# Kernel optimization log

Hardware: AMD Instinct MI355X
Metric: run time of the kernel (lower is better)

The kernel has to match this reference:

```python
import jax, jax.numpy as jnp
import numpy as np
from jax import lax

EPS = 1e-5

def conv2d(x, w, b, pad):
    y = lax.conv_general_dilated(x, w, (1, 1), [(pad, pad), (pad, pad)],
                                 dimension_numbers=('NCHW', 'OIHW', 'NCHW'))
    return y + b[None, :, None, None]

def batchnorm(x, gamma, beta):
    mean = jnp.mean(x, axis=(0, 2, 3), keepdims=True)
    var = jnp.var(x, axis=(0, 2, 3), keepdims=True)  # biased, as torch BN training mode
    return gamma[None, :, None, None] * (x - mean) * lax.rsqrt(var + EPS) + beta[None, :, None, None]

def maxpool2(x):
    return lax.reduce_window(x, -jnp.inf, lax.max, (1, 1, 2, 2), (1, 1, 2, 2), 'VALID')

def upsample(x, s):
    N, C, H, W = x.shape
    return jax.image.resize(x, (N, C, H * s, W * s), method='bilinear')

def select_topvar(x, k=3):
    # per-sample, per-channel unbiased variance; gather top-k variance channels
    N, C, H, W = x.shape
    v = jnp.var(x.reshape(N, C, H * W), axis=-1, ddof=1)  # [N, C]
    _, idx = lax.top_k(v, k)                              # argsort(-v)[:k]
    return jnp.take_along_axis(x, idx[:, :, None, None], axis=1)

def setup_inputs() -> dict:
    key = jax.random.key(0)
    ks = jax.random.split(key, 16)
    n_channel, n_class = 10, 5
    d = {}
    d['x'] = jax.random.normal(ks[0], (16, n_channel, 512, 512), jnp.float32)
    sc = 0.1
    d['w_ext1'] = jax.random.normal(ks[1], (16, n_channel, 1, 1), jnp.float32) * sc
    d['b_ext1'] = jnp.zeros((16,), jnp.float32)
    d['g_ebn1'] = jnp.ones((16,), jnp.float32)
    d['be_ebn1'] = jnp.zeros((16,), jnp.float32)
    d['w_ext2'] = jax.random.normal(ks[2], (16, 16, 1, 1), jnp.float32) * sc
    d['b_ext2'] = jnp.zeros((16,), jnp.float32)
    d['g_ebn2'] = jnp.ones((16,), jnp.float32)
    d['be_ebn2'] = jnp.zeros((16,), jnp.float32)
    d['w_c1'] = jax.random.normal(ks[3], (8, 3, 3, 3), jnp.float32) * sc
    d['b_c1'] = jnp.zeros((8,), jnp.float32)
    d['w_c2'] = jax.random.normal(ks[4], (16, 8, 3, 3), jnp.float32) * sc
    d['b_c2'] = jnp.zeros((16,), jnp.float32)
    d['g_bn1'] = jnp.ones((16,), jnp.float32)
    d['be_bn1'] = jnp.zeros((16,), jnp.float32)
    d['g_bn2'] = jnp.ones((8,), jnp.float32)
    d['be_bn2'] = jnp.zeros((8,), jnp.float32)
    d['w_1k'] = jax.random.normal(ks[5], (n_class, 24, 1, 1), jnp.float32) * sc
    d['b_1k'] = jnp.zeros((n_class,), jnp.float32)
    return d

def reference(x, w_ext1, b_ext1, g_ebn1, be_ebn1, w_ext2, b_ext2, g_ebn2, be_ebn2,
              w_c1, b_c1, w_c2, b_c2, g_bn1, be_bn1, g_bn2, be_bn2, w_1k, b_1k):
    # bandExtract: 1x1 conv -> BN -> sigmoid, twice
    h = jax.nn.sigmoid(batchnorm(conv2d(x, w_ext1, b_ext1, 0), g_ebn1, be_ebn1))
    h = jax.nn.sigmoid(batchnorm(conv2d(h, w_ext2, b_ext2, 0), g_ebn2, be_ebn2))
    # featureSelect: keep 3 channels with largest per-sample variance
    x0 = select_topvar(h, 3)                                   # [N,3,H,W]
    x1 = maxpool2(jax.nn.sigmoid(conv2d(x0, w_c1, b_c1, 1)))   # [N,8,H/2,W/2]
    x2 = maxpool2(jax.nn.sigmoid(conv2d(x1, w_c2, b_c2, 1)))   # [N,16,H/4,W/4]
    x2 = batchnorm(jax.nn.relu(upsample(x2, 4)), g_bn1, be_bn1)  # [N,16,H,W]
    x1 = batchnorm(jax.nn.relu(upsample(x1, 2)), g_bn2, be_bn2)  # [N,8,H,W]
    merge = jnp.concatenate([x1, x2], axis=1)                    # [N,24,H,W]
    return conv2d(merge, w_1k, b_1k, 0)                          # [N,n_class,H,W]
```

## Files before the change

kernel.cpp:

```cpp
#include <hip/hip_runtime.h>
#include <math.h>

#define N_    16
#define CIN_  10
#define CB_   16
#define H_    512
#define W_    512
#define HW_   (512*512)
#define EPSF  1e-5f

__device__ __forceinline__ float sgm(float z){
  float e = __builtin_amdgcn_exp2f(z * -1.44269504088896f);
  return __builtin_amdgcn_rcpf(1.0f + e);
}

__global__ void k_zero(double* __restrict__ p, int n){
  int i = blockIdx.x*256 + threadIdx.x;
  if (i < n) p[i] = 0.0;
}

__global__ void k_fin(const double* __restrict__ S, const float* __restrict__ g,
                      const float* __restrict__ be, float* __restrict__ AB,
                      int C, double invM){
  int c = threadIdx.x;
  if (c < C){
    double s=0.0,q=0.0;
    for (int n=0;n<N_;++n){ s+=S[(n*C+c)*2]; q+=S[(n*C+c)*2+1]; }
    double mean = s*invM;
    double var  = q*invM - mean*mean;
    float a = g[c]*rsqrtf((float)var + EPSF);
    AB[c]   = a;
    AB[C+c] = be[c] - (float)mean*a;
  }
}

__global__ __launch_bounds__(256) void k_cov(
    const float* __restrict__ x, double* __restrict__ SP)
{
  const int n = blockIdx.y;
  const int base = blockIdx.x*4096;
  const float* xp = x + (size_t)n*CIN_*HW_;
  float s[CIN_], p[55];
#pragma unroll
  for (int i=0;i<CIN_;++i) s[i]=0.f;
#pragma unroll
  for (int i=0;i<55;++i) p[i]=0.f;
#pragma unroll 1
  for (int it=0; it<4; ++it){
    const int off = base + it*1024 + threadIdx.x*4;
    float4 xv[CIN_];
#pragma unroll
    for (int ci=0; ci<CIN_; ++ci)
      xv[ci] = *(const float4*)(xp + (size_t)ci*HW_ + off);
#pragma unroll
    for (int ci=0; ci<CIN_; ++ci)
      s[ci] += xv[ci].x + xv[ci].y + xv[ci].z + xv[ci].w;
    int k=0;
#pragma unroll
    for (int i=0;i<CIN_;++i)
#pragma unroll
      for (int j=i;j<CIN_;++j,++k)
        p[k] += xv[i].x*xv[j].x + xv[i].y*xv[j].y + xv[i].z*xv[j].z + xv[i].w*xv[j].w;
  }
  __shared__ float red[4][65];
  const int lane = threadIdx.x & 63, wid = threadIdx.x >> 6;
#pragma unroll
  for (int k=0;k<65;++k){
    float v = (k<CIN_) ? s[k] : p[k-CIN_];
    for (int o=32;o>0;o>>=1) v += __shfl_down(v,o);
    if (lane==0) red[wid][k]=v;
  }
  __syncthreads();
  if (threadIdx.x < 65){
    float v = red[0][threadIdx.x]+red[1][threadIdx.x]+red[2][threadIdx.x]+red[3][threadIdx.x];
    atomicAdd(&SP[n*65+threadIdx.x], (double)v);
  }
}

__global__ void k_fin1(const double* __restrict__ SP, const float* __restrict__ w1,
                       const float* __restrict__ b1, const float* __restrict__ g,
                       const float* __restrict__ be, float* __restrict__ AB){
  __shared__ double Sm[CIN_], Cv[55];
  int t = threadIdx.x;
  if (t < 65){
    double s = 0.0;
    for (int n=0;n<N_;++n) s += SP[n*65+t];
    if (t < CIN_) Sm[t] = s; else Cv[t-CIN_] = s;
  }
  __syncthreads();
  if (t < CB_){
    const double M = 16.0*(double)HW_;
    double b = (double)b1[t];
    double wd[CIN_];
    double lin = 0.0;
    for (int i=0;i<CIN_;++i){ wd[i] = (double)w1[t*CIN_+i]; lin += wd[i]*Sm[i]/M; }
    double mean = b + lin;
    double ey2 = b*b + 2.0*b*lin;
    int k=0;
    for (int i=0;i<CIN_;++i)
      for (int j=i;j<CIN_;++j,++k)
        ey2 += (i==j ? 1.0 : 2.0) * wd[i]*wd[j]*(Cv[k]/M);
    double var = ey2 - mean*mean;
    float a = g[t]*rsqrtf((float)var + EPSF);
    AB[t] = a;
    AB[CB_+t] = be[t] - (float)mean*a;
  }
}

__global__ __launch_bounds__(256) void k_band2(
    const float* __restrict__ x,
    const float* __restrict__ w1, const float* __restrict__ b1, const float* __restrict__ AB1,
    const float* __restrict__ w2, const float* __restrict__ b2,
    float* __restrict__ B, double* __restrict__ S2)
{
  const int n = blockIdx.y;
  const int base = blockIdx.x*4096;
  const float* xp = x + (size_t)n*CIN_*HW_;
  float* bp = B + (size_t)n*CB_*HW_;
  float sum[CB_], sq[CB_];
#pragma unroll
  for (int c=0;c<CB_;++c){ sum[c]=0.f; sq[c]=0.f; }
#pragma unroll 1
  for (int it=0; it<4; ++it){
    const int p = base + it*1024 + threadIdx.x*4;
    float4 xv[CIN_];
#pragma unroll
    for (int ci=0; ci<CIN_; ++ci)
      xv[ci] = *(const float4*)(xp + (size_t)ci*HW_ + p);
    float4 s[CB_];
#pragma unroll
    for (int co=0; co<CB_; ++co){
      float bb = b1[co];
      float ox=bb, oy=bb, oz=bb, ow=bb;
#pragma unroll
      for (int ci=0; ci<CIN_; ++ci){
        float w = w1[co*CIN_+ci];
        ox += w*xv[ci].x; oy += w*xv[ci].y; oz += w*xv[ci].z; ow += w*xv[ci].w;
      }
      const float a = AB1[co], sh = AB1[CB_+co];
      s[co].x = sgm(a*ox+sh); s[co].y = sgm(a*oy+sh);
      s[co].z = sgm(a*oz+sh); s[co].w = sgm(a*ow+sh);
    }
#pragma unroll
    for (int co=0; co<CB_; ++co){
      float bb = b2[co];
      float ox=bb, oy=bb, oz=bb, ow=bb;
#pragma unroll
      for (int ci=0; ci<CB_; ++ci){
        float w = w2[co*CB_+ci];
        ox += w*s[ci].x; oy += w*s[ci].y; oz += w*s[ci].z; ow += w*s[ci].w;
      }
      float4 o; o.x=ox; o.y=oy; o.z=oz; o.w=ow;
      *(float4*)(bp + (size_t)co*HW_ + p) = o;
      sum[co] += ox+oy+oz+ow;
      sq[co]  += ox*ox+oy*oy+oz*oz+ow*ow;
    }
  }
  __shared__ float red[4][CB_][2];
  const int lane = threadIdx.x & 63, wid = threadIdx.x >> 6;
#pragma unroll
  for (int c=0;c<CB_;++c){
    float s=sum[c], q=sq[c];
    for (int off=32; off>0; off>>=1){ s += __shfl_down(s,off); q += __shfl_down(q,off); }
    if (lane==0){ red[wid][c][0]=s; red[wid][c][1]=q; }
  }
  __syncthreads();
  if (threadIdx.x < CB_*2){
    int c = threadIdx.x>>1, k = threadIdx.x&1;
    float t = red[0][c][k]+red[1][c][k]+red[2][c][k]+red[3][c][k];
    atomicAdd(&S2[(n*CB_+c)*2+k], (double)t);
  }
}

__global__ __launch_bounds__(256) void k_varstats(
    const float* __restrict__ B, const float* __restrict__ AB2, double* __restrict__ SV)
{
  const int n = blockIdx.z, c = blockIdx.y;
  const float a = AB2[c], b = AB2[CB_+c];
  const float* p = B + ((size_t)(n*CB_+c))*HW_ + blockIdx.x*4096;
  float sum=0.f, sq=0.f;
#pragma unroll 1
  for (int it=0; it<4; ++it){
    float4 v = *(const float4*)(p + it*1024 + threadIdx.x*4);
    v.x = sgm(a*v.x+b); v.y = sgm(a*v.y+b); v.z = sgm(a*v.z+b); v.w = sgm(a*v.w+b);
    sum += v.x+v.y+v.z+v.w;
    sq  += v.x*v.x+v.y*v.y+v.z*v.z+v.w*v.w;
  }
  __shared__ float red[4][2];
  const int lane = threadIdx.x & 63, wid = threadIdx.x >> 6;
  for (int off=32; off>0; off>>=1){ sum += __shfl_down(sum,off); sq += __shfl_down(sq,off); }
  if (lane==0){ red[wid][0]=sum; red[wid][1]=sq; }
  __syncthreads();
  if (threadIdx.x < 2){
    int k = threadIdx.x;
    float t = red[0][k]+red[1][k]+red[2][k]+red[3][k];
    atomicAdd(&SV[(n*CB_+c)*2+k], (double)t);
  }
}

__global__ void k_topk(const double* __restrict__ SV, int* __restrict__ IDX){
  __shared__ double var[N_][CB_];
  int t = threadIdx.x;
  if (t < N_*CB_){
    int n=t>>4, c=t&15;
    double s=SV[t*2], q=SV[t*2+1];
    const double M = (double)HW_;
    var[n][c] = (q - s*s/M)/(M-1.0);
  }
  __syncthreads();
  if (t < N_){
    double v[CB_];
#pragma unroll
    for (int c=0;c<CB_;++c) v[c]=var[t][c];
    for (int k=0;k<3;++k){
      int bi=0; double bv=v[0];
#pragma unroll
      for (int c=1;c<CB_;++c) if (v[c]>bv){ bv=v[c]; bi=c; }
      IDX[t*3+k]=bi; v[bi]=-1e300;
    }
  }
}

__global__ __launch_bounds__(256) void k_conv1p(
    const float* __restrict__ B, const int* __restrict__ IDX, const float* __restrict__ AB2,
    const float* __restrict__ w, const float* __restrict__ bias,
    float* __restrict__ X1)
{
  const int n = blockIdx.y, ho = blockIdx.x, wo = threadIdx.x;
  __shared__ int chs[3];
  __shared__ float ca[3], cb[3];
  if (threadIdx.x < 3){
    int c = IDX[n*3+threadIdx.x];
    chs[threadIdx.x] = c;
    ca[threadIdx.x] = AB2[c];
    cb[threadIdx.x] = AB2[CB_+c];
  }
  __syncthreads();
  float in[3][4][4];
#pragma unroll
  for (int k=0;k<3;++k){
    const float* pc = B + ((size_t)(n*CB_+chs[k]))*HW_;
    const float a = ca[k], bb = cb[k];
#pragma unroll
    for (int dy=0;dy<4;++dy){
      int r = 2*ho-1+dy;
      bool rok = (r>=0 && r<H_);
#pragma unroll
      for (int dx=0;dx<4;++dx){
        int cc = 2*wo-1+dx;
        in[k][dy][dx] = (rok && cc>=0 && cc<W_) ? sgm(a*pc[(size_t)r*W_+cc]+bb) : 0.f;
      }
    }
  }
#pragma unroll
  for (int co=0;co<8;++co){
    float m = -1e30f;
#pragma unroll
    for (int py=0;py<2;++py)
#pragma unroll
    for (int px=0;px<2;++px){
      float acc = bias[co];
#pragma unroll
      for (int k=0;k<3;++k)
#pragma unroll
      for (int kh=0;kh<3;++kh)
#pragma unroll
      for (int kw=0;kw<3;++kw)
        acc += w[((co*3+k)*3+kh)*3+kw] * in[k][py+kh][px+kw];
      m = fmaxf(m, acc);
    }
    X1[((size_t)(n*8+co)*256 + ho)*256 + wo] = sgm(m);
  }
}

__global__ __launch_bounds__(256) void k_conv2p(
    const float* __restrict__ X1, const float* __restrict__ w, const float* __restrict__ bias,
    float* __restrict__ X2)
{
  const int n  = blockIdx.y;
  const int wo = threadIdx.x & 127;
  const int ho = blockIdx.x*2 + (threadIdx.x>>7);
  float acc[16][4];
#pragma unroll
  for (int co=0;co<16;++co){
    float bb = bias[co];
    acc[co][0]=bb; acc[co][1]=bb; acc[co][2]=bb; acc[co][3]=bb;
  }
#pragma unroll 1
  for (int ci=0; ci<8; ++ci){
    const float* p = X1 + ((size_t)(n*8+ci))*65536;
    float patch[4][4];
#pragma unroll
    for (int dy=0;dy<4;++dy){
      int r = 2*ho-1+dy;
      bool rok = (r>=0 && r<256);
#pragma unroll
      for (int dx=0;dx<4;++dx){
        int cc = 2*wo-1+dx;
        patch[dy][dx] = (rok && cc>=0 && cc<256) ? p[r*256+cc] : 0.f;
      }
    }
#pragma unroll
    for (int co=0;co<16;++co){
      const float* wp = w + (co*8+ci)*9;
#pragma unroll
      for (int py=0;py<2;++py)
#pragma unroll
      for (int px=0;px<2;++px){
        float a = acc[co][py*2+px];
#pragma unroll
        for (int kh=0;kh<3;++kh)
#pragma unroll
        for (int kw=0;kw<3;++kw)
          a += wp[kh*3+kw]*patch[py+kh][px+kw];
        acc[co][py*2+px] = a;
      }
    }
  }
#pragma unroll
  for (int co=0;co<16;++co){
    float m = fmaxf(fmaxf(acc[co][0],acc[co][1]), fmaxf(acc[co][2],acc[co][3]));
    X2[((size_t)(n*16+co)*128 + ho)*128 + wo] = sgm(m);
  }
}

__global__ __launch_bounds__(256) void k_stats_up4(
    const float* __restrict__ X2, double* __restrict__ SB1)
{
  const int n = blockIdx.z, c = blockIdx.y;
  const float* p = X2 + ((size_t)(n*16+c))*16384;
  const int id = blockIdx.x*256 + threadIdx.x;
  const int ho = id>>7, m = id&127;
  const int q = ho>>2, r = ho&3;
  int rA, rB; float wA;
  if (r==0){ rA=q-1; rB=q;   wA=0.375f; }
  else if (r==1){ rA=q-1; rB=q;   wA=0.125f; }
  else if (r==2){ rA=q;   rB=q+1; wA=0.875f; }
  else          { rA=q;   rB=q+1; wA=0.625f; }
  const float wB = 1.f-wA;
  rA = max(rA,0); rB = min(rB,127);
  const int c0 = max(m-1,0), c1 = m, c2 = min(m+1,127);
  const float* pa = p + rA*128; const float* pb = p + rB*128;
  float t0 = wA*pa[c0]+wB*pb[c0];
  float t1 = wA*pa[c1]+wB*pb[c1];
  float t2 = wA*pa[c2]+wB*pb[c2];
  float o0 = fmaxf(0.375f*t0+0.625f*t1, 0.f);
  float o1 = fmaxf(0.125f*t0+0.875f*t1, 0.f);
  float o2 = fmaxf(0.875f*t1+0.125f*t2, 0.f);
  float o3 = fmaxf(0.625f*t1+0.375f*t2, 0.f);
  float sum = o0+o1+o2+o3;
  float sq  = o0*o0+o1*o1+o2*o2+o3*o3;
  __shared__ float red[4][2];
  const int lane = threadIdx.x & 63, wid = threadIdx.x >> 6;
  for (int off=32; off>0; off>>=1){ sum += __shfl_down(sum,off); sq += __shfl_down(sq,off); }
  if (lane==0){ red[wid][0]=sum; red[wid][1]=sq; }
  __syncthreads();
  if (threadIdx.x < 2){
    int k = threadIdx.x;
    float t = red[0][k]+red[1][k]+red[2][k]+red[3][k];
    atomicAdd(&SB1[(n*16+c)*2+k], (double)t);
  }
}

__global__ __launch_bounds__(256) void k_stats_up2(
    const float* __restrict__ X1, double* __restrict__ SB2)
{
  const int n = blockIdx.z, c = blockIdx.y;
  const float* p = X1 + ((size_t)(n*8+c))*65536;
  const int id = blockIdx.x*256 + threadIdx.x;
  const int ho = id>>7, m = id&127;
  const int i = ho>>1, r = ho&1;
  int rA, rB; float wA;
  if (r==0){ rA=i-1; rB=i;   wA=0.25f; }
  else     { rA=i;   rB=i+1; wA=0.75f; }
  const float wB = 1.f-wA;
  rA = max(rA,0); rB = min(rB,255);
  const int c0 = max(2*m-1,0), c1 = 2*m, c2 = 2*m+1, c3 = min(2*m+2,255);
  const float* pa = p + rA*256; const float* pb = p + rB*256;
  float t0 = wA*pa[c0]+wB*pb[c0];
  float t1 = wA*pa[c1]+wB*pb[c1];
  float t2 = wA*pa[c2]+wB*pb[c2];
  float t3 = wA*pa[c3]+wB*pb[c3];
  float o0 = fmaxf(0.25f*t0+0.75f*t1, 0.f);
  float o1 = fmaxf(0.75f*t1+0.25f*t2, 0.f);
  float o2 = fmaxf(0.25f*t1+0.75f*t2, 0.f);
  float o3 = fmaxf(0.75f*t2+0.25f*t3, 0.f);
  float sum = o0+o1+o2+o3;
  float sq  = o0*o0+o1*o1+o2*o2+o3*o3;
  __shared__ float red[4][2];
  const int lane = threadIdx.x & 63, wid = threadIdx.x >> 6;
  for (int off=32; off>0; off>>=1){ sum += __shfl_down(sum,off); sq += __shfl_down(sq,off); }
  if (lane==0){ red[wid][0]=sum; red[wid][1]=sq; }
  __syncthreads();
  if (threadIdx.x < 2){
    int k = threadIdx.x;
    float t = red[0][k]+red[1][k]+red[2][k]+red[3][k];
    atomicAdd(&SB2[(n*8+c)*2+k], (double)t);
  }
}

__global__ __launch_bounds__(256) void k_final(
    const float* __restrict__ X1, const float* __restrict__ X2,
    const float* __restrict__ ABB1, const float* __restrict__ ABB2,
    const float* __restrict__ w1k, const float* __restrict__ b1k,
    float* __restrict__ out)
{
  const int n = blockIdx.y;
  const int id = blockIdx.x*256 + threadIdx.x;
  const int h = id>>7, m = id&127;
  float acc[5][4];
#pragma unroll
  for (int cls=0;cls<5;++cls){
    float bb = b1k[cls];
    acc[cls][0]=bb; acc[cls][1]=bb; acc[cls][2]=bb; acc[cls][3]=bb;
  }
  {
    const int i = h>>1, r = h&1;
    int rA,rB; float wA;
    if (r==0){ rA=i-1; rB=i;   wA=0.25f; } else { rA=i; rB=i+1; wA=0.75f; }
    const float wB = 1.f-wA;
    rA = max(rA,0); rB = min(rB,255);
    const int c0 = max(2*m-1,0), c1 = 2*m, c2 = 2*m+1, c3 = min(2*m+2,255);
#pragma unroll
    for (int c=0;c<8;++c){
      const float* p  = X1 + ((size_t)(n*8+c))*65536;
      const float* pa = p + rA*256; const float* pb = p + rB*256;
      float t0 = wA*pa[c0]+wB*pb[c0];
      float t1 = wA*pa[c1]+wB*pb[c1];
      float t2 = wA*pa[c2]+wB*pb[c2];
      float t3 = wA*pa[c3]+wB*pb[c3];
      float o0 = 0.25f*t0+0.75f*t1, o1 = 0.75f*t1+0.25f*t2;
      float o2 = 0.25f*t1+0.75f*t2, o3 = 0.75f*t2+0.25f*t3;
      const float a = ABB2[c], bb = ABB2[8+c];
      o0 = a*fmaxf(o0,0.f)+bb; o1 = a*fmaxf(o1,0.f)+bb;
      o2 = a*fmaxf(o2,0.f)+bb; o3 = a*fmaxf(o3,0.f)+bb;
#pragma unroll
      for (int cls=0;cls<5;++cls){
        float wv = w1k[cls*24+c];
        acc[cls][0]+=wv*o0; acc[cls][1]+=wv*o1; acc[cls][2]+=wv*o2; acc[cls][3]+=wv*o3;
      }
    }
  }
  {
    const int q = h>>2, r = h&3;
    int rA,rB; float wA;
    if (r==0){ rA=q-1; rB=q;   wA=0.375f; }
    else if (r==1){ rA=q-1; rB=q;   wA=0.125f; }
    else if (r==2){ rA=q;   rB=q+1; wA=0.875f; }
    else          { rA=q;   rB=q+1; wA=0.625f; }
    const float wB = 1.f-wA;
    rA = max(rA,0); rB = min(rB,127);
    const int c0 = max(m-1,0), c1 = m, c2 = min(m+1,127);
#pragma unroll
    for (int c=0;c<16;++c){
      const float* p  = X2 + ((size_t)(n*16+c))*16384;
      const float* pa = p + rA*128; const float* pb = p + rB*128;
      float t0 = wA*pa[c0]+wB*pb[c0];
      float t1 = wA*pa[c1]+wB*pb[c1];
      float t2 = wA*pa[c2]+wB*pb[c2];
      float o0 = 0.375f*t0+0.625f*t1;
      float o1 = 0.125f*t0+0.875f*t1;
      float o2 = 0.875f*t1+0.125f*t2;
      float o3 = 0.625f*t1+0.375f*t2;
      const float a = ABB1[c], bb = ABB1[16+c];
      o0 = a*fmaxf(o0,0.f)+bb; o1 = a*fmaxf(o1,0.f)+bb;
      o2 = a*fmaxf(o2,0.f)+bb; o3 = a*fmaxf(o3,0.f)+bb;
#pragma unroll
      for (int cls=0;cls<5;++cls){
        float wv = w1k[cls*24+8+c];
        acc[cls][0]+=wv*o0; acc[cls][1]+=wv*o1; acc[cls][2]+=wv*o2; acc[cls][3]+=wv*o3;
      }
    }
  }
#pragma unroll
  for (int cls=0;cls<5;++cls){
    float4 v; v.x=acc[cls][0]; v.y=acc[cls][1]; v.z=acc[cls][2]; v.w=acc[cls][3];
    *(float4*)(out + ((size_t)(n*5+cls))*HW_ + (size_t)h*W_ + 4*m) = v;
  }
}

extern "C" void kernel_launch(void* const* d_in, const int* in_sizes, int n_in,
                              void* d_out, int out_size, void* d_ws, size_t ws_size,
                              hipStream_t stream) {
  const float* x       = (const float*)d_in[0];
  const float* w_ext1  = (const float*)d_in[1];
  const float* b_ext1  = (const float*)d_in[2];
  const float* g_ebn1  = (const float*)d_in[3];
  const float* be_ebn1 = (const float*)d_in[4];
  const float* w_ext2  = (const float*)d_in[5];
  const float* b_ext2  = (const float*)d_in[6];
  const float* g_ebn2  = (const float*)d_in[7];
  const float* be_ebn2 = (const float*)d_in[8];
  const float* w_c1    = (const float*)d_in[9];
  const float* b_c1    = (const float*)d_in[10];
  const float* w_c2    = (const float*)d_in[11];
  const float* b_c2    = (const float*)d_in[12];
  const float* g_bn1   = (const float*)d_in[13];
  const float* be_bn1  = (const float*)d_in[14];
  const float* g_bn2   = (const float*)d_in[15];
  const float* be_bn2  = (const float*)d_in[16];
  const float* w_1k    = (const float*)d_in[17];
  const float* b_1k    = (const float*)d_in[18];
  float* outp = (float*)d_out;

  char* ws = (char*)d_ws;
  float* B  = (float*)ws;
  float* X1 = (float*)(ws + 268435456);
  float* X2 = (float*)(ws + 268435456 + 33554432);
  char*  sb = ws + 268435456 + 33554432 + 16777216;
  double* SP  = (double*)sb;
  double* S2  = SP  + 1040;
  double* SV  = S2  + 512;
  double* SB1 = SV  + 512;
  double* SB2 = SB1 + 512;
  float*  AB1  = (float*)(SB2 + 256);
  float*  AB2  = AB1 + 32;
  float*  ABB1 = AB2 + 32;
  float*  ABB2 = ABB1 + 32;
  int*    IDX  = (int*)(ABB2 + 16);

  const double invM_bn = 1.0/4194304.0;

  k_zero<<<12,256,0,stream>>>(SP, 2832);
  k_cov<<<dim3(64,16),256,0,stream>>>(x, SP);
  k_fin1<<<1,128,0,stream>>>(SP, w_ext1, b_ext1, g_ebn1, be_ebn1, AB1);
  k_band2<<<dim3(64,16),256,0,stream>>>(x, w_ext1, b_ext1, AB1, w_ext2, b_ext2, B, S2);
  k_fin<<<1,64,0,stream>>>(S2, g_ebn2, be_ebn2, AB2, 16, invM_bn);
  k_varstats<<<dim3(64,16,16),256,0,stream>>>(B, AB2, SV);
  k_topk<<<1,256,0,stream>>>(SV, IDX);
  k_conv1p<<<dim3(256,16),256,0,stream>>>(B, IDX, AB2, w_c1, b_c1, X1);
  k_conv2p<<<dim3(64,16),256,0,stream>>>(X1, w_c2, b_c2, X2);
  k_stats_up4<<<dim3(256,16,16),256,0,stream>>>(X2, SB1);
  k_stats_up2<<<dim3(256,8,16),256,0,stream>>>(X1, SB2);
  k_fin<<<1,64,0,stream>>>(SB1, g_bn1, be_bn1, ABB1, 16, invM_bn);
  k_fin<<<1,64,0,stream>>>(SB2, g_bn2, be_bn2, ABB2, 8, invM_bn);
  k_final<<<dim3(256,16),256,0,stream>>>(X1, X2, ABB1, ABB2, w_1k, b_1k, outp);
}
```

Baseline: 813.7 us.

## Scalarize band kernel with more blocks and stage conv1 input rows in LDS

k_band2 now processes one pixel per thread per iteration instead of a float4, and the grid grows from 64 to 256 blocks per sample. This is meant to cut register pressure and raise occupancy and parallelism, at the cost of narrower scalar loads and stores. k_conv1p now loads each needed input row once into a shared-memory tile, applying the sigmoid once per element. This removes the redundant overlapping 4x4 loads and sigmoid evaluations each thread did before, and adds a barrier and explicit zero padding at the tile edges.

```diff
diff --git a/kernel.cpp b/kernel.cpp
--- a/kernel.cpp
+++ b/kernel.cpp
@@ -114,7 +114,7 @@
     float* __restrict__ B, double* __restrict__ S2)
 {
   const int n = blockIdx.y;
-  const int base = blockIdx.x*4096;
+  const int base = blockIdx.x*1024;
   const float* xp = x + (size_t)n*CIN_*HW_;
   float* bp = B + (size_t)n*CB_*HW_;
   float sum[CB_], sq[CB_];
@@ -122,38 +122,29 @@
   for (int c=0;c<CB_;++c){ sum[c]=0.f; sq[c]=0.f; }
 #pragma unroll 1
   for (int it=0; it<4; ++it){
-    const int p = base + it*1024 + threadIdx.x*4;
-    float4 xv[CIN_];
+    const int p = base + it*256 + threadIdx.x;
+    float xv[CIN_];
 #pragma unroll
     for (int ci=0; ci<CIN_; ++ci)
-      xv[ci] = *(const float4*)(xp + (size_t)ci*HW_ + p);
-    float4 s[CB_];
+      xv[ci] = xp[(size_t)ci*HW_ + p];
+    float s[CB_];
 #pragma unroll
     for (int co=0; co<CB_; ++co){
-      float bb = b1[co];
-      float ox=bb, oy=bb, oz=bb, ow=bb;
-#pragma unroll
-      for (int ci=0; ci<CIN_; ++ci){
-        float w = w1[co*CIN_+ci];
-        ox += w*xv[ci].x; oy += w*xv[ci].y; oz += w*xv[ci].z; ow += w*xv[ci].w;
-      }
-      const float a = AB1[co], sh = AB1[CB_+co];
-      s[co].x = sgm(a*ox+sh); s[co].y = sgm(a*oy+sh);
-      s[co].z = sgm(a*oz+sh); s[co].w = sgm(a*ow+sh);
+      float o = b1[co];
+#pragma unroll
+      for (int ci=0; ci<CIN_; ++ci)
+        o += w1[co*CIN_+ci]*xv[ci];
+      s[co] = sgm(AB1[co]*o + AB1[CB_+co]);
     }
 #pragma unroll
     for (int co=0; co<CB_; ++co){
-      float bb = b2[co];
-      float ox=bb, oy=bb, oz=bb, ow=bb;
-#pragma unroll
-      for (int ci=0; ci<CB_; ++ci){
-        float w = w2[co*CB_+ci];
-        ox += w*s[ci].x; oy += w*s[ci].y; oz += w*s[ci].z; ow += w*s[ci].w;
-      }
-      float4 o; o.x=ox; o.y=oy; o.z=oz; o.w=ow;
-      *(float4*)(bp + (size_t)co*HW_ + p) = o;
-      sum[co] += ox+oy+oz+ow;
-      sq[co]  += ox*ox+oy*oy+oz*oz+ow*ow;
+      float o = b2[co];
+#pragma unroll
+      for (int ci=0; ci<CB_; ++ci)
+        o += w2[co*CB_+ci]*s[ci];
+      bp[(size_t)co*HW_ + p] = o;
+      sum[co] += o;
+      sq[co]  += o*o;
     }
   }
   __shared__ float red[4][CB_][2];
@@ -227,6 +218,7 @@
     float* __restrict__ X1)
 {
   const int n = blockIdx.y, ho = blockIdx.x, wo = threadIdx.x;
+  __shared__ float tile[3][4][516];
   __shared__ int chs[3];
   __shared__ float ca[3], cb[3];
   if (threadIdx.x < 3){
@@ -236,22 +228,35 @@
     cb[threadIdx.x] = AB2[CB_+c];
   }
   __syncthreads();
-  float in[3][4][4];
 #pragma unroll
   for (int k=0;k<3;++k){
     const float* pc = B + ((size_t)(n*CB_+chs[k]))*HW_;
     const float a = ca[k], bb = cb[k];
 #pragma unroll
     for (int dy=0;dy<4;++dy){
-      int r = 2*ho-1+dy;
-      bool rok = (r>=0 && r<H_);
-#pragma unroll
-      for (int dx=0;dx<4;++dx){
-        int cc = 2*wo-1+dx;
-        in[k][dy][dx] = (rok && cc>=0 && cc<W_) ? sgm(a*pc[(size_t)r*W_+cc]+bb) : 0.f;
+      const int r = 2*ho-1+dy;
+      float tx = 0.f, ty = 0.f;
+      if (r>=0 && r<H_){
+        const float2 v = *(const float2*)(pc + (size_t)r*W_ + 2*wo);
+        tx = sgm(a*v.x+bb); ty = sgm(a*v.y+bb);
       }
-    }
-  }
+      tile[k][dy][1+2*wo] = tx;
+      tile[k][dy][2+2*wo] = ty;
+    }
+  }
+  if (wo < 24){
+    int k = wo>>3, dy = (wo&7)>>1;
+    tile[k][dy][(wo&1) ? 513 : 0] = 0.f;
+  }
+  __syncthreads();
+  float in[3][4][4];
+#pragma unroll
+  for (int k=0;k<3;++k)
+#pragma unroll
+    for (int dy=0;dy<4;++dy)
+#pragma unroll
+      for (int dx=0;dx<4;++dx)
+        in[k][dy][dx] = tile[k][dy][2*wo+dx];
 #pragma unroll
   for (int co=0;co<8;++co){
     float m = -1e30f;
@@ -524,7 +529,7 @@
   k_zero<<<12,256,0,stream>>>(SP, 2832);
   k_cov<<<dim3(64,16),256,0,stream>>>(x, SP);
   k_fin1<<<1,128,0,stream>>>(SP, w_ext1, b_ext1, g_ebn1, be_ebn1, AB1);
-  k_band2<<<dim3(64,16),256,0,stream>>>(x, w_ext1, b_ext1, AB1, w_ext2, b_ext2, B, S2);
+  k_band2<<<dim3(256,16),256,0,stream>>>(x, w_ext1, b_ext1, AB1, w_ext2, b_ext2, B, S2);
   k_fin<<<1,64,0,stream>>>(S2, g_ebn2, be_ebn2, AB2, 16, invM_bn);
   k_varstats<<<dim3(64,16,16),256,0,stream>>>(B, AB2, SV);
   k_topk<<<1,256,0,stream>>>(SV, IDX);
```

Result: no change. 800.1 us (-1.7%).

## Stage conv1 input rows and final upsample source rows in shared memory

Applied to the files above, without the earlier changes.

k_conv1p now loads each input row once per block with float2 loads, applies the BN+sigmoid once per element, stores the result in a shared tile with zero-padded edges, and then reads the 4x4 windows from LDS. Before, each thread recomputed the sigmoid for overlapping neighbours. k_final now has each block cooperatively load the X1 and X2 rows it needs into shared memory, so the per-thread gathered global loads for bilinear upsampling become LDS reads. The cost is extra LDS use and barriers, which may lower occupancy.

```diff
diff --git a/kernel.cpp b/kernel.cpp
--- a/kernel.cpp
+++ b/kernel.cpp
@@ -227,6 +227,7 @@
     float* __restrict__ X1)
 {
   const int n = blockIdx.y, ho = blockIdx.x, wo = threadIdx.x;
+  __shared__ float tile[3][4][516];
   __shared__ int chs[3];
   __shared__ float ca[3], cb[3];
   if (threadIdx.x < 3){
@@ -236,22 +237,35 @@
     cb[threadIdx.x] = AB2[CB_+c];
   }
   __syncthreads();
-  float in[3][4][4];
 #pragma unroll
   for (int k=0;k<3;++k){
     const float* pc = B + ((size_t)(n*CB_+chs[k]))*HW_;
     const float a = ca[k], bb = cb[k];
 #pragma unroll
     for (int dy=0;dy<4;++dy){
-      int r = 2*ho-1+dy;
-      bool rok = (r>=0 && r<H_);
-#pragma unroll
-      for (int dx=0;dx<4;++dx){
-        int cc = 2*wo-1+dx;
-        in[k][dy][dx] = (rok && cc>=0 && cc<W_) ? sgm(a*pc[(size_t)r*W_+cc]+bb) : 0.f;
-      }
-    }
-  }
+      const int r = 2*ho-1+dy;
+      float tx = 0.f, ty = 0.f;
+      if (r>=0 && r<H_){
+        const float2 v = *(const float2*)(pc + (size_t)r*W_ + 2*wo);
+        tx = sgm(a*v.x+bb); ty = sgm(a*v.y+bb);
+      }
+      tile[k][dy][1+2*wo] = tx;
+      tile[k][dy][2+2*wo] = ty;
+    }
+  }
+  if (wo < 24){
+    int k = wo>>3, dy = (wo&7)>>1;
+    tile[k][dy][(wo&1) ? 513 : 0] = 0.f;
+  }
+  __syncthreads();
+  float in[3][4][4];
+#pragma unroll
+  for (int k=0;k<3;++k)
+#pragma unroll
+    for (int dy=0;dy<4;++dy)
+#pragma unroll
+      for (int dx=0;dx<4;++dx)
+        in[k][dy][dx] = tile[k][dy][2*wo+dx];
 #pragma unroll
   for (int co=0;co<8;++co){
     float m = -1e30f;
@@ -405,9 +419,35 @@
     const float* __restrict__ w1k, const float* __restrict__ b1k,
     float* __restrict__ out)
 {
-  const int n = blockIdx.y;
-  const int id = blockIdx.x*256 + threadIdx.x;
-  const int h = id>>7, m = id&127;
+  const int n = blockIdx.y, bx = blockIdx.x, tid = threadIdx.x;
+  __shared__ float sx1[8][3][256];
+  __shared__ float sx2[16][2][128];
+  {
+    const int R0 = max(bx-1,0), R1 = bx, R2 = min(bx+1,255);
+#pragma unroll
+    for (int pr=0; pr<24; ++pr){
+      const int ch = pr/3, row = pr%3;
+      const int rr = (row==0) ? R0 : ((row==1) ? R1 : R2);
+      sx1[ch][row][tid] = X1[((size_t)(n*8+ch)*256 + rr)*256 + tid];
+    }
+  }
+  {
+    const int q = bx>>1;
+    const int Q0 = (bx&1) ? q : max(q-1,0);
+    const int Q1 = (bx&1) ? min(q+1,127) : q;
+    const int col = tid & 127, half = tid >> 7;
+#pragma unroll
+    for (int k=0;k<16;++k){
+      const int pr = half + 2*k;
+      const int ch = pr>>1, row = pr&1;
+      const int rr = row ? Q1 : Q0;
+      sx2[ch][row][col] = X2[((size_t)(n*16+ch)*128 + rr)*128 + col];
+    }
+  }
+  __syncthreads();
+
+  const int h = 2*bx + (tid>>7);
+  const int m = tid & 127;
   float acc[5][4];
 #pragma unroll
   for (int cls=0;cls<5;++cls){
@@ -415,16 +455,15 @@
     acc[cls][0]=bb; acc[cls][1]=bb; acc[cls][2]=bb; acc[cls][3]=bb;
   }
   {
-    const int i = h>>1, r = h&1;
-    int rA,rB; float wA;
-    if (r==0){ rA=i-1; rB=i;   wA=0.25f; } else { rA=i; rB=i+1; wA=0.75f; }
+    const int r = h&1;
+    const float wA = (r==0) ? 0.25f : 0.75f;
     const float wB = 1.f-wA;
-    rA = max(rA,0); rB = min(rB,255);
+    const int paL = r, pbL = r+1;
     const int c0 = max(2*m-1,0), c1 = 2*m, c2 = 2*m+1, c3 = min(2*m+2,255);
 #pragma unroll
     for (int c=0;c<8;++c){
-      const float* p  = X1 + ((size_t)(n*8+c))*65536;
-      const float* pa = p + rA*256; const float* pb = p + rB*256;
+      const float* pa = &sx1[c][paL][0];
+      const float* pb = &sx1[c][pbL][0];
       float t0 = wA*pa[c0]+wB*pb[c0];
       float t1 = wA*pa[c1]+wB*pb[c1];
       float t2 = wA*pa[c2]+wB*pb[c2];
@@ -442,19 +481,18 @@
     }
   }
   {
-    const int q = h>>2, r = h&3;
-    int rA,rB; float wA;
-    if (r==0){ rA=q-1; rB=q;   wA=0.375f; }
-    else if (r==1){ rA=q-1; rB=q;   wA=0.125f; }
-    else if (r==2){ rA=q;   rB=q+1; wA=0.875f; }
-    else          { rA=q;   rB=q+1; wA=0.625f; }
+    const int r = h&3;
+    float wA;
+    if (r==0)      wA=0.375f;
+    else if (r==1) wA=0.125f;
+    else if (r==2) wA=0.875f;
+    else           wA=0.625f;
     const float wB = 1.f-wA;
-    rA = max(rA,0); rB = min(rB,127);
     const int c0 = max(m-1,0), c1 = m, c2 = min(m+1,127);
 #pragma unroll
     for (int c=0;c<16;++c){
-      const float* p  = X2 + ((size_t)(n*16+c))*16384;
-      const float* pa = p + rA*128; const float* pb = p + rB*128;
+      const float* pa = &sx2[c][0][0];
+      const float* pb = &sx2[c][1][0];
       float t0 = wA*pa[c0]+wB*pb[c0];
       float t1 = wA*pa[c1]+wB*pb[c1];
       float t2 = wA*pa[c2]+wB*pb[c2];
```

Result: no change. 800.3 us (-1.7%).
